# Kernel optimization log

Measured on AMD Instinct MI355X. Metric: run time of the kernel, lower is better.

Reference implementation:

```python
import jax, jax.numpy as jnp
import numpy as np

DIM = 512
CODEBOOK_SIZE = 8192


def setup_inputs() -> dict:
    key = jax.random.key(0)
    k_x, k_e = jax.random.split(key)
    x = jax.random.normal(k_x, (4, 4096, DIM), dtype=jnp.float32)
    # EuclideanCodebook buffer: embed ~ randn(codebook_size, dim)
    embed = jax.random.normal(k_e, (CODEBOOK_SIZE, DIM), dtype=jnp.float32)
    return {"x": x, "embed": embed}


def reference(x, embed):
    # projection_in / projection_out are Identity (codebook_dim=None)
    shape = x.shape
    flatten = x.reshape(-1, shape[-1])  # [N, D]
    # dist = -(||f||^2 - 2 f @ e^T + ||e||^2)  -> negative squared euclidean
    f_sq = jnp.sum(flatten * flatten, axis=1, keepdims=True)          # [N, 1]
    e_sq = jnp.sum(embed * embed, axis=1)[None, :]                    # [1, K]
    dist = -(f_sq - 2.0 * flatten @ embed.T + e_sq)                   # [N, K]
    embed_ind = jnp.argmax(dist, axis=-1)                             # [N]
    embed_ind = embed_ind.reshape(shape[:-1])                         # [B, S]
    quantize = jnp.take(embed, embed_ind, axis=0)                     # [B, S, D]
    return quantize, embed_ind
```

## Files before the change

kernel.cpp:

```cpp
#include <hip/hip_runtime.h>

#define DIM    512
#define KCODES 8192
#define NROWS  16384
#define NEG_INF -3.402823466e38f
#define MARGIN 2.0f
#define CPR 128

typedef unsigned short ushort_t;
typedef unsigned int uint_t;
typedef __attribute__((ext_vector_type(4))) int   v4i;
typedef __attribute__((ext_vector_type(4))) float v4f;

__device__ inline void dma16(const void* g, void* l) {
    __builtin_amdgcn_global_load_lds(
        (const __attribute__((address_space(1))) unsigned int*)g,
        (__attribute__((address_space(3))) unsigned int*)l, 16, 0, 0);
}

__global__ __launch_bounds__(512) void convert_kernel(
    const float* __restrict__ x, const float* __restrict__ embed,
    int4* __restrict__ e_t8, int4* __restrict__ x_t8,
    float* __restrict__ e_sq, float* __restrict__ esqh,
    float* __restrict__ f_sq,
    float* __restrict__ e_scale, float* __restrict__ f_scale)
{
    __shared__ __align__(16) char buf[64][528];

    const int w = threadIdx.x >> 6;
    const int lane = threadIdx.x & 63;
    const bool isE = blockIdx.x < (KCODES / 64);
    const int rows0 = isE ? blockIdx.x * 64 : (blockIdx.x - KCODES / 64) * 64;
    const float* src_base = isE ? embed : x;

    #pragma unroll
    for (int rr = 0; rr < 8; ++rr) {
        int r_local = w * 8 + rr;
        const float* src = src_base + (size_t)(rows0 + r_local) * DIM + lane * 8;
        float4 a = *(const float4*)src;
        float4 b = *(const float4*)(src + 4);
        float s = a.x*a.x + a.y*a.y + a.z*a.z + a.w*a.w
                + b.x*b.x + b.y*b.y + b.z*b.z + b.w*b.w;
        float am = fmaxf(fmaxf(fmaxf(fabsf(a.x), fabsf(a.y)), fmaxf(fabsf(a.z), fabsf(a.w))),
                         fmaxf(fmaxf(fabsf(b.x), fabsf(b.y)), fmaxf(fabsf(b.z), fabsf(b.w))));
        #pragma unroll
        for (int off = 32; off >= 1; off >>= 1) {
            s += __shfl_xor(s, off, 64);
            am = fmaxf(am, __shfl_xor(am, off, 64));
        }
        float inv = (am > 0.0f) ? 127.0f / am : 0.0f;

        float vq[8] = {a.x, a.y, a.z, a.w, b.x, b.y, b.z, b.w};
        uint_t lo = 0, hi = 0;
        #pragma unroll
        for (int jj = 0; jj < 4; ++jj) {
            lo |= ((uint_t)((int)rintf(vq[jj]     * inv) & 0xff)) << (8 * jj);
            hi |= ((uint_t)((int)rintf(vq[4 + jj] * inv) & 0xff)) << (8 * jj);
        }
        *(int*)&buf[r_local][8 * lane]     = (int)lo;
        *(int*)&buf[r_local][8 * lane + 4] = (int)hi;

        if (lane == 0) {
            int r = rows0 + r_local;
            float sc = am * (1.0f / 127.0f);
            if (isE) { e_sq[r] = s; esqh[r] = -0.5f * s; e_scale[r] = sc; }
            else     { f_sq[r] = s; f_scale[r] = sc; }
        }
    }
    __syncthreads();

    #pragma unroll
    for (int i = 0; i < 4; ++i) {
        int sq = w * 4 + i;
        int4 v = *(const int4*)&buf[lane][16 * sq];
        if (isE) e_t8[(size_t)sq * KCODES + rows0 + lane] = v;
        else     x_t8[(size_t)sq * NROWS  + rows0 + lane] = v;
    }
}

__global__ __launch_bounds__(1024, 4) void screen_kernel(
    const int4* __restrict__ e_t8, const int4* __restrict__ x_t8,
    const float* __restrict__ esqh,
    const float* __restrict__ e_scale, const float* __restrict__ f_scale,
    float* __restrict__ cand_s, int* __restrict__ cand_i)
{
    __shared__ __align__(16) char EH[2][8][256][16];
    __shared__ __align__(16) char XH[2][8][256][16];

    const int t = threadIdx.x;
    const int w = t >> 6;
    const int lane = t & 63;
    const int quad = lane >> 4;
    const int l15 = lane & 15;
    const int wm = w & 3;
    const int wn = w >> 2;

    const int n = blockIdx.x;
    const int xcd = n & 7;
    const int j = n >> 3;
    const int rt = xcd * 8 + (j & 7);
    const int ct = j >> 3;
    const int row0 = rt * 256;
    const int cbase = ct * 256;

    const bool isE = w < 8;
    const int qp = isE ? w : (w - 8);
    const int4* gbase = isE ? (e_t8 + cbase + lane)
                            : (x_t8 + row0 + lane);
    const size_t gstride = isE ? KCODES : NROWS;

    v4i acc[4][4];
    #pragma unroll
    for (int mi = 0; mi < 4; ++mi)
        #pragma unroll
        for (int nj = 0; nj < 4; ++nj)
            acc[mi][nj] = (v4i){0, 0, 0, 0};

    auto issue_dma = [&](int S) {
        int buf = S & 1;
        char* ldst = isE ? &EH[buf][qp][0][0] : &XH[buf][qp][0][0];
        size_t soff = (size_t)(S * 8 + qp) * gstride;
        #pragma unroll
        for (int i = 0; i < 4; ++i)
            dma16(gbase + soff + i * 64, ldst + i * 64 * 16);
    };

    issue_dma(0);

    for (int S = 0; S < 4; ++S) {
        __syncthreads();
        if (S < 3) issue_dma(S + 1);
        const int buf = S & 1;

        #pragma unroll
        for (int ks = 0; ks < 2; ++ks) {
            const int q = ks * 4 + quad;
            v4i bh[4];
            #pragma unroll
            for (int nj = 0; nj < 4; ++nj)
                bh[nj] = *(const v4i*)(&XH[buf][q][wn * 64 + nj * 16 + l15][0]);
            #pragma unroll
            for (int mi = 0; mi < 4; ++mi) {
                v4i ah = *(const v4i*)(&EH[buf][q][wm * 64 + mi * 16 + l15][0]);
                #pragma unroll
                for (int nj = 0; nj < 4; ++nj)
                    acc[mi][nj] = __builtin_amdgcn_mfma_i32_16x16x64_i8(ah, bh[nj], acc[mi][nj], 0, 0, 0);
            }
        }
    }

    __syncthreads();
    float* scr_s = (float*)&EH[0][0][0][0];
    int*   scr_i = (int*)  &XH[0][0][0][0];

    #pragma unroll
    for (int nj = 0; nj < 4; ++nj) {
        float sfv = f_scale[row0 + wn * 64 + nj * 16 + l15];
        float b1 = NEG_INF, b2 = NEG_INF;
        int   i1 = 0x7fffffff, i2 = 0x7fffffff;
        #pragma unroll
        for (int mi = 0; mi < 4; ++mi) {
            v4f se4 = *(const v4f*)(e_scale + cbase + wm * 64 + mi * 16 + quad * 4);
            v4f eq4 = *(const v4f*)(esqh    + cbase + wm * 64 + mi * 16 + quad * 4);
            int cid0 = cbase + wm * 64 + mi * 16 + quad * 4;
            #pragma unroll
            for (int jj = 0; jj < 4; ++jj) {
                float sc = fmaf(sfv * se4[jj], (float)acc[mi][nj][jj], eq4[jj]);
                int cc = cid0 + jj;
                if (sc > b1)      { b2 = b1; i2 = i1; b1 = sc; i1 = cc; }
                else if (sc > b2) { b2 = sc; i2 = cc; }
            }
        }
        #pragma unroll
        for (int o = 16; o <= 32; o <<= 1) {
            float c1 = __shfl_xor(b1, o, 64);
            int   j1 = __shfl_xor(i1, o, 64);
            float c2 = __shfl_xor(b2, o, 64);
            int   j2 = __shfl_xor(i2, o, 64);
            if (c1 > b1) {
                b2 = fmaxf(b1, c2); i2 = (b1 >= c2) ? i1 : j2;
                b1 = c1; i1 = j1;
            } else {
                i2 = (b2 >= c1) ? i2 : j1;
                b2 = fmaxf(b2, c1);
            }
        }
        if (quad == 0) {
            int rl = wn * 64 + nj * 16 + l15;
            int base = (wm * 256 + rl) * 2;
            scr_s[base]     = b1;  scr_i[base]     = i1;
            scr_s[base + 1] = b2;  scr_i[base + 1] = i2;
        }
    }
    __syncthreads();

    if (t < 512) {
        int rl = t >> 1;
        int pr = t & 1;
        int ba = ((2 * pr) * 256 + rl) * 2;
        int bb = ((2 * pr + 1) * 256 + rl) * 2;
        float a1 = scr_s[ba], a2 = scr_s[ba + 1];
        int   ia = scr_i[ba], i2a = scr_i[ba + 1];
        float c1 = scr_s[bb], c2 = scr_s[bb + 1];
        int   ic = scr_i[bb], i2c = scr_i[bb + 1];
        float b1, b2; int j1, j2;
        if (a1 >= c1) {
            b1 = a1; j1 = ia;
            if (a2 >= c1) { b2 = a2; j2 = i2a; } else { b2 = c1; j2 = ic; }
        } else {
            b1 = c1; j1 = ic;
            if (c2 >= a1) { b2 = c2; j2 = i2c; } else { b2 = a1; j2 = ia; }
        }
        size_t b = (size_t)(row0 + rl) * CPR + (ct * 4 + pr * 2);
        cand_s[b]     = b1;  cand_i[b]     = j1;
        cand_s[b + 1] = b2;  cand_i[b + 1] = j2;
    }
}

__global__ __launch_bounds__(256) void rescore_kernel(
    const float* __restrict__ x, const float* __restrict__ embed,
    const float* __restrict__ e_sq, const float* __restrict__ f_sq,
    const float* __restrict__ cand_s, const int* __restrict__ cand_i,
    float* __restrict__ out)
{
    int row = blockIdx.x * 4 + (threadIdx.x >> 6);
    int lane = threadIdx.x & 63;
    size_t cb = (size_t)row * CPR;

    float cs0 = cand_s[cb + lane];
    float cs1 = cand_s[cb + 64 + lane];
    int   ci0 = cand_i[cb + lane];
    int   ci1 = cand_i[cb + 64 + lane];

    float m = fmaxf(cs0, cs1);
    #pragma unroll
    for (int o = 32; o >= 1; o >>= 1) m = fmaxf(m, __shfl_xor(m, o, 64));

    unsigned long long mask0 = __ballot(cs0 >= m - MARGIN);
    unsigned long long mask1 = __ballot(cs1 >= m - MARGIN);

    const float4* xsrc = (const float4*)(x + (size_t)row * DIM + lane * 8);
    float4 xa = xsrc[0], xb = xsrc[1];
    float fsq = f_sq[row];

    float bd = NEG_INF;
    int   bi = 0x7fffffff;

    #pragma unroll
    for (int s = 0; s < 2; ++s) {
        unsigned long long mask = s ? mask1 : mask0;
        while (mask) {
            int p = __ffsll(mask) - 1;
            mask &= mask - 1;
            int c = __shfl(s ? ci1 : ci0, p);
            const float4* er = (const float4*)(embed + (size_t)c * DIM + lane * 8);
            float4 ea = er[0], eb = er[1];
            float part = xa.x*ea.x + xa.y*ea.y + xa.z*ea.z + xa.w*ea.w
                       + xb.x*eb.x + xb.y*eb.y + xb.z*eb.z + xb.w*eb.w;
            #pragma unroll
            for (int o = 32; o >= 1; o >>= 1) part += __shfl_xor(part, o, 64);
            float d = -((fsq - 2.0f * part) + e_sq[c]);
            if (d > bd || (d == bd && c < bi)) { bd = d; bi = c; }
        }
    }

    const float4* er = (const float4*)(embed + (size_t)bi * DIM + lane * 8);
    float4 qa = er[0], qb = er[1];
    float4* dst = (float4*)(out + (size_t)row * DIM + lane * 8);
    dst[0] = qa; dst[1] = qb;
    if (lane == 0) out[(size_t)NROWS * DIM + row] = (float)bi;
}

extern "C" void kernel_launch(void* const* d_in, const int* in_sizes, int n_in,
                              void* d_out, int out_size, void* d_ws, size_t ws_size,
                              hipStream_t stream)
{
    const float* x     = (const float*)d_in[0];
    const float* embed = (const float*)d_in[1];
    float* out = (float*)d_out;

    float* e_sq    = (float*)d_ws;
    float* esqh    = e_sq + KCODES;
    float* f_sq    = esqh + KCODES;
    float* e_scale = f_sq + NROWS;
    float* f_scale = e_scale + KCODES;
    float* cand_s  = f_scale + NROWS;
    int*   cand_i  = (int*)(cand_s + (size_t)NROWS * CPR);
    int4*  e_t8    = (int4*)(cand_i + (size_t)NROWS * CPR);

    int4* x_t8 = (int4*)d_out;

    (void)in_sizes; (void)n_in; (void)out_size; (void)ws_size;

    convert_kernel<<<(KCODES + NROWS) / 64, 512, 0, stream>>>(
        x, embed, e_t8, x_t8, e_sq, esqh, f_sq, e_scale, f_scale);
    screen_kernel<<<2048, 1024, 0, stream>>>(
        e_t8, x_t8, esqh, e_scale, f_scale, cand_s, cand_i);
    rescore_kernel<<<NROWS / 4, 256, 0, stream>>>(
        x, embed, e_sq, f_sq, cand_s, cand_i, out);
}
```

Before: 236.3 us.

## Shrink screen tiles to 128x128 with 4-wave blocks and MFMA priority

The int8 screening GEMM moves from 256x256 tiles with 16-wave blocks to 128x128 tiles with 4-wave blocks. Each wave now loads both E and X slices, the K loop runs 8 stages of 64 bytes, and the grid grows to 8192 blocks. s_setprio is raised around the MFMA section. Each 128-code tile now writes 2 candidates per row instead of 4 per 256 codes, so CPR=128 is still filled. The aim is better occupancy, finer load balance and lower per-block LDS use, at the cost of more global reloads from smaller tile reuse and more barriers per block.

```diff
diff --git a/kernel.cpp b/kernel.cpp
--- a/kernel.cpp
+++ b/kernel.cpp
@@ -78,36 +78,33 @@
     }
 }
 
-__global__ __launch_bounds__(1024, 4) void screen_kernel(
+__global__ __launch_bounds__(256, 3) void screen_kernel(
     const int4* __restrict__ e_t8, const int4* __restrict__ x_t8,
     const float* __restrict__ esqh,
     const float* __restrict__ e_scale, const float* __restrict__ f_scale,
     float* __restrict__ cand_s, int* __restrict__ cand_i)
 {
-    __shared__ __align__(16) char EH[2][8][256][16];
-    __shared__ __align__(16) char XH[2][8][256][16];
+    __shared__ __align__(16) char EH[2][4][128][16];
+    __shared__ __align__(16) char XH[2][4][128][16];
 
     const int t = threadIdx.x;
     const int w = t >> 6;
     const int lane = t & 63;
     const int quad = lane >> 4;
     const int l15 = lane & 15;
-    const int wm = w & 3;
-    const int wn = w >> 2;
+    const int wm = w & 1;
+    const int wn = w >> 1;
 
     const int n = blockIdx.x;
     const int xcd = n & 7;
-    const int j = n >> 3;
-    const int rt = xcd * 8 + (j & 7);
-    const int ct = j >> 3;
-    const int row0 = rt * 256;
-    const int cbase = ct * 256;
-
-    const bool isE = w < 8;
-    const int qp = isE ? w : (w - 8);
-    const int4* gbase = isE ? (e_t8 + cbase + lane)
-                            : (x_t8 + row0 + lane);
-    const size_t gstride = isE ? KCODES : NROWS;
+    const int m = n >> 3;
+    const int ct = xcd * 8 + (m & 7);
+    const int rt = m >> 3;
+    const int row0 = rt * 128;
+    const int cbase = ct * 128;
+
+    const int4* ep = e_t8 + cbase + lane;
+    const int4* xp = x_t8 + row0 + lane;
 
     v4i acc[4][4];
     #pragma unroll
@@ -118,35 +115,33 @@
 
     auto issue_dma = [&](int S) {
         int buf = S & 1;
-        char* ldst = isE ? &EH[buf][qp][0][0] : &XH[buf][qp][0][0];
-        size_t soff = (size_t)(S * 8 + qp) * gstride;
-        #pragma unroll
-        for (int i = 0; i < 4; ++i)
-            dma16(gbase + soff + i * 64, ldst + i * 64 * 16);
+        size_t sq = (size_t)(S * 4 + w);
+        dma16(ep + sq * KCODES,      &EH[buf][w][0][0]);
+        dma16(ep + sq * KCODES + 64, &EH[buf][w][64][0]);
+        dma16(xp + sq * NROWS,       &XH[buf][w][0][0]);
+        dma16(xp + sq * NROWS + 64,  &XH[buf][w][64][0]);
     };
 
     issue_dma(0);
 
-    for (int S = 0; S < 4; ++S) {
+    for (int S = 0; S < 8; ++S) {
         __syncthreads();
-        if (S < 3) issue_dma(S + 1);
+        if (S < 7) issue_dma(S + 1);
         const int buf = S & 1;
 
-        #pragma unroll
-        for (int ks = 0; ks < 2; ++ks) {
-            const int q = ks * 4 + quad;
-            v4i bh[4];
+        v4i bh[4];
+        #pragma unroll
+        for (int nj = 0; nj < 4; ++nj)
+            bh[nj] = *(const v4i*)(&XH[buf][quad][wn * 64 + nj * 16 + l15][0]);
+        __builtin_amdgcn_s_setprio(1);
+        #pragma unroll
+        for (int mi = 0; mi < 4; ++mi) {
+            v4i ah = *(const v4i*)(&EH[buf][quad][wm * 64 + mi * 16 + l15][0]);
             #pragma unroll
             for (int nj = 0; nj < 4; ++nj)
-                bh[nj] = *(const v4i*)(&XH[buf][q][wn * 64 + nj * 16 + l15][0]);
-            #pragma unroll
-            for (int mi = 0; mi < 4; ++mi) {
-                v4i ah = *(const v4i*)(&EH[buf][q][wm * 64 + mi * 16 + l15][0]);
-                #pragma unroll
-                for (int nj = 0; nj < 4; ++nj)
-                    acc[mi][nj] = __builtin_amdgcn_mfma_i32_16x16x64_i8(ah, bh[nj], acc[mi][nj], 0, 0, 0);
-            }
-        }
+                acc[mi][nj] = __builtin_amdgcn_mfma_i32_16x16x64_i8(ah, bh[nj], acc[mi][nj], 0, 0, 0);
+        }
+        __builtin_amdgcn_s_setprio(0);
     }
 
     __syncthreads();
@@ -187,18 +182,17 @@
         }
         if (quad == 0) {
             int rl = wn * 64 + nj * 16 + l15;
-            int base = (wm * 256 + rl) * 2;
+            int base = (wm * 128 + rl) * 2;
             scr_s[base]     = b1;  scr_i[base]     = i1;
             scr_s[base + 1] = b2;  scr_i[base + 1] = i2;
         }
     }
     __syncthreads();
 
-    if (t < 512) {
-        int rl = t >> 1;
-        int pr = t & 1;
-        int ba = ((2 * pr) * 256 + rl) * 2;
-        int bb = ((2 * pr + 1) * 256 + rl) * 2;
+    if (t < 128) {
+        int rl = t;
+        int ba = rl * 2;
+        int bb = (128 + rl) * 2;
         float a1 = scr_s[ba], a2 = scr_s[ba + 1];
         int   ia = scr_i[ba], i2a = scr_i[ba + 1];
         float c1 = scr_s[bb], c2 = scr_s[bb + 1];
@@ -211,7 +205,7 @@
             b1 = c1; j1 = ic;
             if (c2 >= a1) { b2 = c2; j2 = i2c; } else { b2 = a1; j2 = ia; }
         }
-        size_t b = (size_t)(row0 + rl) * CPR + (ct * 4 + pr * 2);
+        size_t b = (size_t)(row0 + rl) * CPR + (size_t)(ct * 2);
         cand_s[b]     = b1;  cand_i[b]     = j1;
         cand_s[b + 1] = b2;  cand_i[b + 1] = j2;
     }
@@ -294,7 +288,7 @@
 
     convert_kernel<<<(KCODES + NROWS) / 64, 512, 0, stream>>>(
         x, embed, e_t8, x_t8, e_sq, esqh, f_sq, e_scale, f_scale);
-    screen_kernel<<<2048, 1024, 0, stream>>>(
+    screen_kernel<<<8192, 256, 0, stream>>>(
         e_t8, x_t8, esqh, e_scale, f_scale, cand_s, cand_i);
     rescore_kernel<<<NROWS / 4, 256, 0, stream>>>(
         x, embed, e_sq, f_sq, cand_s, cand_i, out);
```

After: 229.4 us. -2.9%, faster.
